# Performance work log

Measured on AMD Instinct MI355X. Metric: run time of the kernel, lower is better.

## Reference

```python
import jax, jax.numpy as jnp
import numpy as np

N_NODES = 100000
N_EDGES = 400000
N_GRAPHS = 2000
NODE_F = 78
HID = 128


def gcn_conv(x, src, dst, W, b, n_nodes):
    # PyG GCNConv: h = X @ W; add self-loops; symmetric norm; scatter-add; + bias
    h = x @ W
    loop = jnp.arange(n_nodes, dtype=src.dtype)
    s = jnp.concatenate([src, loop])
    d = jnp.concatenate([dst, loop])
    deg = jax.ops.segment_sum(jnp.ones_like(d, dtype=h.dtype), d, num_segments=n_nodes)
    dinv = jax.lax.rsqrt(deg)  # deg >= 1 due to self-loops
    coef = dinv[s] * dinv[d]  # [E+N]
    msg = h[s] * coef[:, None]  # gather + scale
    out = jax.ops.segment_sum(msg, d, num_segments=n_nodes)
    return out + b


def setup_inputs() -> dict:
    key = jax.random.key(0)
    ks = jax.random.split(key, 16)
    x = jax.random.normal(ks[0], (N_NODES, NODE_F), dtype=jnp.float32)
    edge_index = jax.random.randint(ks[1], (2, N_EDGES), 0, N_NODES, dtype=jnp.int64)
    batch = jnp.sort(jax.random.randint(ks[2], (N_NODES,), 0, N_GRAPHS, dtype=jnp.int64))
    def lin(k, fi, fo):
        lim = 1.0 / np.sqrt(fi)
        kw, kb = jax.random.split(k)
        return (jax.random.uniform(kw, (fi, fo), jnp.float32, -lim, lim),
                jax.random.uniform(kb, (fo,), jnp.float32, -lim, lim))
    W1, b1 = lin(ks[3], NODE_F, HID)
    W2, b2 = lin(ks[4], HID, 2 * HID)
    W3, b3 = lin(ks[5], 2 * HID, HID)
    fw1, fb1 = lin(ks[6], HID, 64)
    fw2, fb2 = lin(ks[7], 64, 1)
    return {"x": x, "edge_index": edge_index, "batch": batch,
            "W1": W1, "b1": b1, "W2": W2, "b2": b2, "W3": W3, "b3": b3,
            "fw1": fw1, "fb1": fb1, "fw2": fw2, "fb2": fb2}


def reference(x, edge_index, batch, W1, b1, W2, b2, W3, b3, fw1, fb1, fw2, fb2):
    src, dst = edge_index[0], edge_index[1]
    h = jax.nn.relu(gcn_conv(x, src, dst, W1, b1, N_NODES))
    h = jax.nn.relu(gcn_conv(h, src, dst, W2, b2, N_NODES))
    h = jax.nn.relu(gcn_conv(h, src, dst, W3, b3, N_NODES))
    # global_mean_pool over graph ids
    sums = jax.ops.segment_sum(h, batch, num_segments=N_GRAPHS)
    cnts = jax.ops.segment_sum(jnp.ones((N_NODES,), h.dtype), batch, num_segments=N_GRAPHS)
    pooled = sums / jnp.maximum(cnts, 1.0)[:, None]
    h = jax.nn.relu(pooled @ fw1 + fb1)
    return h @ fw2 + fb2  # [N_GRAPHS, 1]
```

## Files before the change

kernel.cpp:

```cpp
#include <hip/hip_runtime.h>

#define N_NODES 100000
#define N_EDGES 400000
#define N_GRAPHS 2000
#define NODE_F 78
#define HID 128
#define PAD 32
#define SENT N_NODES

typedef __attribute__((ext_vector_type(8))) short short8v;
typedef __attribute__((ext_vector_type(4))) float f32x4;

__device__ __forceinline__ ushort f2bf(float f) {
    unsigned u = __float_as_uint(f);
    unsigned r = (u + 0x7FFFu + ((u >> 16) & 1u)) >> 16;
    return (ushort)r;
}
__device__ __forceinline__ float bf2f(ushort b) {
    return __uint_as_float(((unsigned)b) << 16);
}
__device__ __forceinline__ float2 bfx2(const ushort* p) {
    unsigned u = *reinterpret_cast<const unsigned*>(p);
    return make_float2(__uint_as_float(u << 16), __uint_as_float(u & 0xffff0000u));
}
__device__ __forceinline__ unsigned packbf(float a, float b) {
    return (unsigned)f2bf(a) | ((unsigned)f2bf(b) << 16);
}
__device__ __forceinline__ void gload16(const ushort* g, ushort* l) {
    __builtin_amdgcn_global_load_lds((const __attribute__((address_space(1))) unsigned int*)g,
                                     (__attribute__((address_space(3))) unsigned int*)l, 16, 0, 0);
}


__global__ void setup_k(int* __restrict__ cursor, int4* __restrict__ csr4,
                        ushort* __restrict__ xb, ushort* __restrict__ b1,
                        ushort* __restrict__ b3) {
    int i = blockIdx.x * blockDim.x + threadIdx.x;
    if (i < N_NODES * PAD / 4) csr4[i] = make_int4(SENT, SENT, SENT, SENT);
    if (i < N_NODES) cursor[i] = 0;
    if (i < 80) xb[(size_t)N_NODES * 80 + i] = 0;
    if (i < 128) {
        b1[(size_t)N_NODES * 128 + i] = 0;
        b3[(size_t)N_NODES * 128 + i] = 0;
    }
}

__global__ void fill_csr_k(const int* __restrict__ src, const int* __restrict__ dst,
                           int* __restrict__ cursor, int* __restrict__ csr) {
    int e = blockIdx.x * blockDim.x + threadIdx.x;
    if (e >= N_EDGES) return;
    int s = src[e], d = dst[e];
    int p = atomicAdd(&cursor[d], 1);
    if (p < PAD) csr[d * PAD + p] = s;
}

__global__ void dinv_k(const int* __restrict__ deg, float* __restrict__ dinv, int n) {
    int i = blockIdx.x * blockDim.x + threadIdx.x;
    if (i < n) dinv[i] = rsqrtf((float)deg[i] + 1.0f);
}


__global__ void x2bf_k(const float* __restrict__ x, const float* __restrict__ dinv,
                       ushort* __restrict__ xb) {
    int idx = blockIdx.x * blockDim.x + threadIdx.x;
    if (idx >= N_NODES * 80) return;
    int n = idx / 80, f = idx - n * 80;
    xb[idx] = (f < NODE_F) ? f2bf(x[(long long)n * NODE_F + f] * dinv[n]) : (ushort)0;
}


__global__ void prep_wt_k(const float* __restrict__ W, ushort* __restrict__ Wth,
                          int K, int N) {
    int idx = blockIdx.x * blockDim.x + threadIdx.x;
    if (idx >= N * 256) return;
    int n = idx >> 8, k = idx & 255;
    Wth[idx] = (k < K) ? f2bf(W[(long long)k * N + n]) : (ushort)0;
}

__global__ void prep_w2img_k(const float* __restrict__ W2, ushort* __restrict__ img) {
    int idx = blockIdx.x * blockDim.x + threadIdx.x;
    if (idx >= 256 * 128) return;
    int n = idx >> 7, k = idx & 127;
    int c = k >> 3;
    int slot = (c & 8) | ((c & 7) ^ (n & 7));
    img[n * 128 + slot * 8 + (k & 7)] = f2bf(W2[(long long)k * 256 + n]);
}

__global__ void prep_w3img_k(const float* __restrict__ W3, ushort* __restrict__ img) {
    int idx = blockIdx.x * blockDim.x + threadIdx.x;
    if (idx >= 128 * 256) return;
    int n = idx >> 8, k = idx & 255;
    int ch = k >> 6, cc = (k >> 3) & 7;
    img[ch * 8192 + n * 64 + ((cc ^ (n & 7)) * 8) + (k & 7)] = f2bf(W3[(long long)k * 128 + n]);
}


__global__ __launch_bounds__(256) void gemm1_k(
        const ushort* __restrict__ A, int M,
        const ushort* __restrict__ Wth, const float* __restrict__ bias,
        const float* __restrict__ dinv, ushort* __restrict__ C) {
    __shared__ ushort At[128 * 64];
    __shared__ ushort Bh[128 * 64];
    const int tid = threadIdx.x;
    const int w = tid >> 6, l = tid & 63;
    const int bm = blockIdx.x * 128;

    f32x4 acc[2][8];
    #pragma unroll
    for (int m = 0; m < 2; ++m)
        #pragma unroll
        for (int j = 0; j < 8; ++j)
            acc[m][j] = (f32x4){0.f, 0.f, 0.f, 0.f};

    for (int k0 = 0; k0 < 128; k0 += 64) {
        __syncthreads();
        #pragma unroll
        for (int i = 0; i < 4; ++i) {
            int idx = tid + i * 256;
            int r = idx >> 3, s0 = idx & 7;
            int gr = bm + r; if (gr >= M) gr = M - 1;
            int kk = k0 + s0 * 8;
            short8v v;
            if (kk < 80) v = *reinterpret_cast<const short8v*>(&A[(size_t)gr * 80 + kk]);
            else v = (short8v){0,0,0,0,0,0,0,0};
            *reinterpret_cast<short8v*>(&At[r * 64 + (s0 ^ (r & 7)) * 8]) = v;
        }
        #pragma unroll
        for (int i = 0; i < 4; ++i) {
            int idx = tid + i * 256;
            int n = idx >> 3, s0 = idx & 7;
            long long g = (long long)n * 256 + k0 + s0 * 8;
            *reinterpret_cast<short8v*>(&Bh[n * 64 + (s0 ^ (n & 7)) * 8]) =
                *reinterpret_cast<const short8v*>(&Wth[g]);
        }
        __syncthreads();
        #pragma unroll
        for (int ks = 0; ks < 2; ++ks) {
            short8v ah[2];
            #pragma unroll
            for (int m = 0; m < 2; ++m) {
                int r = w * 32 + m * 16 + (l & 15);
                ah[m] = *reinterpret_cast<const short8v*>(
                    &At[r * 64 + ((ks * 4 + (l >> 4)) ^ (r & 7)) * 8]);
            }
            #pragma unroll
            for (int j = 0; j < 8; ++j) {
                int n = j * 16 + (l & 15);
                short8v bh = *reinterpret_cast<const short8v*>(
                    &Bh[n * 64 + ((ks * 4 + (l >> 4)) ^ (n & 7)) * 8]);
                #pragma unroll
                for (int m = 0; m < 2; ++m)
                    acc[m][j] = __builtin_amdgcn_mfma_f32_16x16x32_bf16(ah[m], bh, acc[m][j], 0, 0, 0);
            }
        }
    }

    float dv[2][4];
    #pragma unroll
    for (int m = 0; m < 2; ++m)
        #pragma unroll
        for (int rg = 0; rg < 4; ++rg) {
            int gr = bm + w * 32 + m * 16 + (l >> 4) * 4 + rg;
            dv[m][rg] = (gr < M) ? dinv[gr] : 0.f;
        }
    #pragma unroll
    for (int j = 0; j < 8; ++j) {
        int gc = j * 16 + (l & 15);
        float bv = bias[gc];
        #pragma unroll
        for (int m = 0; m < 2; ++m) {
            #pragma unroll
            for (int rg = 0; rg < 4; ++rg) {
                int gr = bm + w * 32 + m * 16 + (l >> 4) * 4 + rg;
                if (gr < M)
                    C[(size_t)gr * 128 + gc] = f2bf(fmaxf(acc[m][j][rg] + bv, 0.0f) * dv[m][rg]);
            }
        }
    }
}


__global__ __launch_bounds__(512) void gemm23_k(
        const ushort* __restrict__ A,
        const ushort* __restrict__ W2i, const float* __restrict__ b2,
        const ushort* __restrict__ W3i, const float* __restrict__ dinv,
        ushort* __restrict__ C, int M) {
    __shared__ ushort At[128 * 128];
    __shared__ ushort Wb[2][8192];
    __shared__ ushort Tb[8][1024];
    const int tid = threadIdx.x;
    const int w = tid >> 6, l = tid & 63;
    const int bm = blockIdx.x * 128;

    {
        const ushort* asrc = A + (size_t)bm * 128;
        #pragma unroll
        for (int i = 0; i < 4; ++i) {
            int chunk = w * 4 + i;
            gload16(asrc + chunk * 512 + l * 8, &At[chunk * 512]);
        }
        #pragma unroll
        for (int i = 0; i < 2; ++i) {
            int chunk = w * 2 + i;
            gload16(W2i + chunk * 512 + l * 8, &Wb[0][chunk * 512]);
        }
    }
    __syncthreads();

    f32x4 acc2[16];
    #pragma unroll
    for (int j = 0; j < 16; ++j) acc2[j] = (f32x4){0.f, 0.f, 0.f, 0.f};

    #pragma unroll
    for (int q = 0; q < 4; ++q) {
        const ushort* nsrc = (q < 3) ? (W2i + (q + 1) * 8192) : W3i;
        #pragma unroll
        for (int i = 0; i < 2; ++i) {
            int chunk = w * 2 + i;
            gload16(nsrc + chunk * 512 + l * 8, &Wb[(q + 1) & 1][chunk * 512]);
        }
        const ushort* wb = Wb[q & 1];
        #pragma unroll
        for (int ks = 0; ks < 4; ++ks) {
            int r = w * 16 + (l & 15);
            int ck = ks * 4 + (l >> 4);
            int sa = (ck & 8) | ((ck & 7) ^ (r & 7));
            short8v ah = *reinterpret_cast<const short8v*>(&At[r * 128 + sa * 8]);
            #pragma unroll
            for (int jt = 0; jt < 4; ++jt) {
                int n = jt * 16 + (l & 15);
                int sb = (ck & 8) | ((ck & 7) ^ (n & 7));
                short8v bh = *reinterpret_cast<const short8v*>(&wb[n * 128 + sb * 8]);
                acc2[q * 4 + jt] = __builtin_amdgcn_mfma_f32_16x16x32_bf16(ah, bh, acc2[q * 4 + jt], 0, 0, 0);
            }
        }
        __syncthreads();
    }

    f32x4 acc3[8];
    #pragma unroll
    for (int j = 0; j < 8; ++j) acc3[j] = (f32x4){0.f, 0.f, 0.f, 0.f};

    #pragma unroll
    for (int ch = 0; ch < 4; ++ch) {
        if (ch < 3) {
            const ushort* nsrc = W3i + (ch + 1) * 8192;
            #pragma unroll
            for (int i = 0; i < 2; ++i) {
                int chunk = w * 2 + i;
                gload16(nsrc + chunk * 512 + l * 8, &Wb[(ch + 1) & 1][chunk * 512]);
            }
        }
        #pragma unroll
        for (int jj = 0; jj < 4; ++jj) {
            int j = ch * 4 + jj;
            float bv = b2[ch * 64 + jj * 16 + (l & 15)];
            #pragma unroll
            for (int rg = 0; rg < 4; ++rg) {
                int rr = (l >> 4) * 4 + rg;
                int cl = jj * 16 + (l & 15);
                Tb[w][rr * 64 + (((cl >> 3) ^ (rr & 7)) * 8) + (cl & 7)] =
                    f2bf(fmaxf(acc2[j][rg] + bv, 0.f));
            }
        }
        const ushort* wb = Wb[ch & 1];
        #pragma unroll
        for (int ks = 0; ks < 2; ++ks) {
            int rt = l & 15;
            int ck = ks * 4 + (l >> 4);
            short8v ah = *reinterpret_cast<const short8v*>(&Tb[w][rt * 64 + ((ck ^ (rt & 7)) * 8)]);
            #pragma unroll
            for (int j3 = 0; j3 < 8; ++j3) {
                int n = j3 * 16 + (l & 15);
                short8v bh = *reinterpret_cast<const short8v*>(&wb[n * 64 + ((ck ^ (n & 7)) * 8)]);
                acc3[j3] = __builtin_amdgcn_mfma_f32_16x16x32_bf16(ah, bh, acc3[j3], 0, 0, 0);
            }
        }
        __syncthreads();
    }

    float dv[4];
    #pragma unroll
    for (int rg = 0; rg < 4; ++rg) {
        int gr = bm + w * 16 + (l >> 4) * 4 + rg;
        dv[rg] = (gr < M) ? dinv[gr] : 0.f;
    }
    #pragma unroll
    for (int j = 0; j < 8; ++j) {
        int gc = j * 16 + (l & 15);
        #pragma unroll
        for (int rg = 0; rg < 4; ++rg) {
            int gr = bm + w * 16 + (l >> 4) * 4 + rg;
            if (gr < M) C[(size_t)gr * 128 + gc] = f2bf(acc3[j][rg] * dv[rg]);
        }
    }
}


__global__ __launch_bounds__(256) void gather78_k(const ushort* __restrict__ Xb,
        const int* __restrict__ deg, const int* __restrict__ csr,
        const float* __restrict__ dinv, ushort* __restrict__ out) {
    int wid = (blockIdx.x * blockDim.x + threadIdx.x) >> 6;
    int lane = threadIdx.x & 63;
    if (wid >= N_NODES) return;
    float di = dinv[wid];
    float ax = 0.f, ay = 0.f;
    bool act = lane < 40;
    if (act) {
        float2 v = bfx2(&Xb[(size_t)wid * 80 + lane * 2]);
        ax = v.x; ay = v.y;
    }
    int d = deg[wid]; if (d > PAD) d = PAD;
    const int4* e4 = reinterpret_cast<const int4*>(csr + wid * PAD);
    for (int j0 = 0; j0 < d; j0 += 4) {
        int4 e = e4[j0 >> 2];
        if (act) {
            float2 v0 = bfx2(&Xb[(size_t)e.x * 80 + lane * 2]);
            float2 v1 = bfx2(&Xb[(size_t)e.y * 80 + lane * 2]);
            float2 v2 = bfx2(&Xb[(size_t)e.z * 80 + lane * 2]);
            float2 v3 = bfx2(&Xb[(size_t)e.w * 80 + lane * 2]);
            ax += v0.x + v1.x + v2.x + v3.x;
            ay += v0.y + v1.y + v2.y + v3.y;
        }
    }
    if (act)
        *reinterpret_cast<unsigned*>(&out[(size_t)wid * 80 + lane * 2]) = packbf(ax * di, ay * di);
}

__global__ __launch_bounds__(256) void gather128_k(const ushort* __restrict__ A,
        const int* __restrict__ deg, const int* __restrict__ csr,
        const float* __restrict__ dinv, ushort* __restrict__ out) {
    int wid = (blockIdx.x * blockDim.x + threadIdx.x) >> 6;
    int lane = threadIdx.x & 63;
    if (wid >= N_NODES) return;
    float di = dinv[wid];
    float2 v = bfx2(&A[(size_t)wid * 128 + lane * 2]);
    float ax = v.x, ay = v.y;
    int d = deg[wid]; if (d > PAD) d = PAD;
    const int4* e4 = reinterpret_cast<const int4*>(csr + wid * PAD);
    for (int j0 = 0; j0 < d; j0 += 4) {
        int4 e = e4[j0 >> 2];
        float2 w0 = bfx2(&A[(size_t)e.x * 128 + lane * 2]);
        float2 w1 = bfx2(&A[(size_t)e.y * 128 + lane * 2]);
        float2 w2 = bfx2(&A[(size_t)e.z * 128 + lane * 2]);
        float2 w3 = bfx2(&A[(size_t)e.w * 128 + lane * 2]);
        ax += w0.x + w1.x + w2.x + w3.x;
        ay += w0.y + w1.y + w2.y + w3.y;
    }
    int kt = lane >> 5, cc = (lane >> 2) & 7, q4 = lane & 3;
    int slot = kt * 8 + (cc ^ (wid & 7));
    *reinterpret_cast<unsigned*>(&out[(size_t)wid * 128 + slot * 8 + q4 * 2]) = packbf(ax * di, ay * di);
}


__global__ __launch_bounds__(512) void pool_head_k(
        const ushort* __restrict__ A,
        const int* __restrict__ deg, const int* __restrict__ csr,
        const float* __restrict__ dinv, const float* __restrict__ b3,
        const int* __restrict__ batch,
        const float* __restrict__ fw1, const float* __restrict__ fb1,
        const float* __restrict__ fw2, const float* __restrict__ fb2,
        float* __restrict__ out) {
    __shared__ float part[8][HID];
    __shared__ float ps[HID];
    const int g = blockIdx.x;
    const int w = threadIdx.x >> 6, lane = threadIdx.x & 63;

    int start, end;
    {
        int l = 0, h = N_NODES;
        while (l < h) { int m = (l + h) >> 1; if (batch[m] < g) l = m + 1; else h = m; }
        start = l;
        h = N_NODES;
        while (l < h) { int m = (l + h) >> 1; if (batch[m] < g + 1) l = m + 1; else h = m; }
        end = l;
    }

    float sx = 0.f, sy = 0.f;
    const float bx = b3[lane * 2], by = b3[lane * 2 + 1];
    for (int i = start + w; i < end; i += 8) {
        float di = dinv[i];
        float2 v = bfx2(&A[(size_t)i * 128 + lane * 2]);
        float ax = v.x, ay = v.y;
        int d = deg[i]; if (d > PAD) d = PAD;
        const int4* e4 = reinterpret_cast<const int4*>(csr + i * PAD);
        for (int j0 = 0; j0 < d; j0 += 4) {
            int4 e = e4[j0 >> 2];
            float2 w0 = bfx2(&A[(size_t)e.x * 128 + lane * 2]);
            float2 w1 = bfx2(&A[(size_t)e.y * 128 + lane * 2]);
            float2 w2 = bfx2(&A[(size_t)e.z * 128 + lane * 2]);
            float2 w3 = bfx2(&A[(size_t)e.w * 128 + lane * 2]);
            ax += w0.x + w1.x + w2.x + w3.x;
            ay += w0.y + w1.y + w2.y + w3.y;
        }
        sx += fmaxf(ax * di + bx, 0.f);
        sy += fmaxf(ay * di + by, 0.f);
    }
    part[w][lane * 2] = sx;
    part[w][lane * 2 + 1] = sy;
    __syncthreads();

    if (w == 0) {
        float inv = (end > start) ? 1.0f / (float)(end - start) : 0.0f;
        float s0 = 0.f, s1 = 0.f;
        #pragma unroll
        for (int q = 0; q < 8; ++q) {
            s0 += part[q][lane * 2];
            s1 += part[q][lane * 2 + 1];
        }
        ps[lane * 2] = s0 * inv;
        ps[lane * 2 + 1] = s1 * inv;
    }
    __syncthreads();

    if (w == 0) {
        float acc = fb1[lane];
        #pragma unroll 8
        for (int k = 0; k < HID; ++k) acc = fmaf(ps[k], fw1[k * 64 + lane], acc);
        float v = fmaxf(acc, 0.0f) * fw2[lane];
        #pragma unroll
        for (int off = 32; off > 0; off >>= 1) v += __shfl_down(v, off);
        if (lane == 0) out[g] = v + fb2[0];
    }
}


extern "C" void kernel_launch(void* const* d_in, const int* in_sizes, int n_in,
                              void* d_out, int out_size, void* d_ws, size_t ws_size,
                              hipStream_t stream) {
    const float* x     = (const float*)d_in[0];
    const int*   ei    = (const int*)d_in[1];
    const int*   batch = (const int*)d_in[2];
    const float* W1 = (const float*)d_in[3];
    const float* b1 = (const float*)d_in[4];
    const float* W2 = (const float*)d_in[5];
    const float* b2 = (const float*)d_in[6];
    const float* W3 = (const float*)d_in[7];
    const float* b3 = (const float*)d_in[8];
    const float* fw1 = (const float*)d_in[9];
    const float* fb1 = (const float*)d_in[10];
    const float* fw2 = (const float*)d_in[11];
    const float* fb2 = (const float*)d_in[12];
    float* out = (float*)d_out;

    const int* src = ei;
    const int* dst = ei + N_EDGES;

    char* p = (char*)d_ws;
    float*  dinv  = (float*)p;  p += 100352 * 4;
    int*    cur   = (int*)p;    p += 100352 * 4;
    int*    csr   = (int*)p;    p += (size_t)N_NODES * PAD * 4;
    ushort* w1h   = (ushort*)p; p += 256 * 256 * 2;
    ushort* img2  = (ushort*)p; p += 256 * 128 * 2;
    ushort* img3  = (ushort*)p; p += 128 * 256 * 2;
    ushort* xb    = (ushort*)p; p += (size_t)(N_NODES + 1) * 80 * 2;
    ushort* xpadb = (ushort*)p; p += (size_t)N_NODES * 80 * 2;
    ushort* buf1  = (ushort*)p; p += (size_t)(N_NODES + 1) * 128 * 2;
    ushort* buf2  = (ushort*)p; p += (size_t)N_NODES * 128 * 2;
    ushort* buf3  = (ushort*)p; p += (size_t)(N_NODES + 1) * 128 * 2;

    const int T = 256;
    const int gw = (N_NODES * 64 + T - 1) / T;

    setup_k<<<(N_NODES * PAD / 4 + T - 1) / T, T, 0, stream>>>(cur, (int4*)csr, xb, buf1, buf3);
    fill_csr_k<<<(N_EDGES + T - 1) / T, T, 0, stream>>>(src, dst, cur, csr);
    dinv_k<<<(N_NODES + T - 1) / T, T, 0, stream>>>(cur, dinv, N_NODES);
    x2bf_k<<<(N_NODES * 80 + T - 1) / T, T, 0, stream>>>(x, dinv, xb);

    prep_wt_k<<<(128 * 256 + T - 1) / T, T, 0, stream>>>(W1, w1h, NODE_F, 128);
    prep_w2img_k<<<(256 * 128 + T - 1) / T, T, 0, stream>>>(W2, img2);
    prep_w3img_k<<<(128 * 256 + T - 1) / T, T, 0, stream>>>(W3, img3);

    gather78_k<<<gw, T, 0, stream>>>(xb, cur, csr, dinv, xpadb);
    gemm1_k<<<782, 256, 0, stream>>>(xpadb, N_NODES, w1h, b1, dinv, buf1);

    gather128_k<<<gw, T, 0, stream>>>(buf1, cur, csr, dinv, buf2);
    gemm23_k<<<782, 512, 0, stream>>>(buf2, img2, b2, img3, dinv, buf3, N_NODES);

    pool_head_k<<<N_GRAPHS, 512, 0, stream>>>(buf3, cur, csr, dinv, b3, batch,
                                              fw1, fb1, fw2, fb2, out);
}
```

Before: 308.9 us.

## Fuse neighbor gather aggregation into GEMM kernels, removing intermediate buffers

```diff
diff --git a/kernel.cpp b/kernel.cpp
--- a/kernel.cpp
+++ b/kernel.cpp
@@ -69,12 +69,13 @@
 }
 
 
-__global__ void prep_wt_k(const float* __restrict__ W, ushort* __restrict__ Wth,
-                          int K, int N) {
+__global__ void prep_w1img_k(const float* __restrict__ W1, ushort* __restrict__ img) {
     int idx = blockIdx.x * blockDim.x + threadIdx.x;
-    if (idx >= N * 256) return;
-    int n = idx >> 8, k = idx & 255;
-    Wth[idx] = (k < K) ? f2bf(W[(long long)k * N + n]) : (ushort)0;
+    if (idx >= 128 * 128) return;
+    int n = idx >> 7, k = idx & 127;
+    int c = k >> 3;
+    int slot = (c & 8) | ((c & 7) ^ (n & 7));
+    img[n * 128 + slot * 8 + (k & 7)] = (k < NODE_F) ? f2bf(W1[(long long)k * 128 + n]) : (ushort)0;
 }
 
 __global__ void prep_w2img_k(const float* __restrict__ W2, ushort* __restrict__ img) {
@@ -95,96 +96,96 @@
 }
 
 
-__global__ __launch_bounds__(256) void gemm1_k(
-        const ushort* __restrict__ A, int M,
-        const ushort* __restrict__ Wth, const float* __restrict__ bias,
-        const float* __restrict__ dinv, ushort* __restrict__ C) {
-    __shared__ ushort At[128 * 64];
-    __shared__ ushort Bh[128 * 64];
+__global__ __launch_bounds__(512) void gemm1g_k(
+        const ushort* __restrict__ Xb, const int* __restrict__ deg,
+        const int* __restrict__ csr, const float* __restrict__ dinv,
+        const ushort* __restrict__ W1i, const float* __restrict__ bias,
+        ushort* __restrict__ C, int M) {
+    __shared__ ushort At[128 * 128];
+    __shared__ ushort Bh[128 * 128];
     const int tid = threadIdx.x;
     const int w = tid >> 6, l = tid & 63;
     const int bm = blockIdx.x * 128;
 
-    f32x4 acc[2][8];
-    #pragma unroll
-    for (int m = 0; m < 2; ++m)
-        #pragma unroll
-        for (int j = 0; j < 8; ++j)
-            acc[m][j] = (f32x4){0.f, 0.f, 0.f, 0.f};
-
-    for (int k0 = 0; k0 < 128; k0 += 64) {
-        __syncthreads();
-        #pragma unroll
-        for (int i = 0; i < 4; ++i) {
-            int idx = tid + i * 256;
-            int r = idx >> 3, s0 = idx & 7;
-            int gr = bm + r; if (gr >= M) gr = M - 1;
-            int kk = k0 + s0 * 8;
-            short8v v;
-            if (kk < 80) v = *reinterpret_cast<const short8v*>(&A[(size_t)gr * 80 + kk]);
-            else v = (short8v){0,0,0,0,0,0,0,0};
-            *reinterpret_cast<short8v*>(&At[r * 64 + (s0 ^ (r & 7)) * 8]) = v;
-        }
-        #pragma unroll
-        for (int i = 0; i < 4; ++i) {
-            int idx = tid + i * 256;
-            int n = idx >> 3, s0 = idx & 7;
-            long long g = (long long)n * 256 + k0 + s0 * 8;
-            *reinterpret_cast<short8v*>(&Bh[n * 64 + (s0 ^ (n & 7)) * 8]) =
-                *reinterpret_cast<const short8v*>(&Wth[g]);
-        }
-        __syncthreads();
-        #pragma unroll
-        for (int ks = 0; ks < 2; ++ks) {
-            short8v ah[2];
-            #pragma unroll
-            for (int m = 0; m < 2; ++m) {
-                int r = w * 32 + m * 16 + (l & 15);
-                ah[m] = *reinterpret_cast<const short8v*>(
-                    &At[r * 64 + ((ks * 4 + (l >> 4)) ^ (r & 7)) * 8]);
+    #pragma unroll
+    for (int i = 0; i < 4; ++i) {
+        int chunk = i * 8 + w;
+        gload16(W1i + chunk * 512 + l * 8, &Bh[chunk * 512]);
+    }
+
+    const bool act = l < 40;
+    for (int t = 0; t < 16; ++t) {
+        int r = w * 16 + t;
+        int gr = bm + r; if (gr >= M) gr = M - 1;
+        float di = dinv[gr];
+        int d = deg[gr]; if (d > PAD) d = PAD;
+        const int4* e4 = reinterpret_cast<const int4*>(csr + gr * PAD);
+        float ax = 0.f, ay = 0.f;
+        if (act) {
+            float2 v = bfx2(&Xb[(size_t)gr * 80 + l * 2]);
+            ax = v.x; ay = v.y;
+        }
+        for (int j0 = 0; j0 < d; j0 += 4) {
+            int4 e = e4[j0 >> 2];
+            if (act) {
+                float2 v0 = bfx2(&Xb[(size_t)e.x * 80 + l * 2]);
+                float2 v1 = bfx2(&Xb[(size_t)e.y * 80 + l * 2]);
+                float2 v2 = bfx2(&Xb[(size_t)e.z * 80 + l * 2]);
+                float2 v3 = bfx2(&Xb[(size_t)e.w * 80 + l * 2]);
+                ax += v0.x + v1.x + v2.x + v3.x;
+                ay += v0.y + v1.y + v2.y + v3.y;
             }
-            #pragma unroll
-            for (int j = 0; j < 8; ++j) {
-                int n = j * 16 + (l & 15);
-                short8v bh = *reinterpret_cast<const short8v*>(
-                    &Bh[n * 64 + ((ks * 4 + (l >> 4)) ^ (n & 7)) * 8]);
-                #pragma unroll
-                for (int m = 0; m < 2; ++m)
-                    acc[m][j] = __builtin_amdgcn_mfma_f32_16x16x32_bf16(ah[m], bh, acc[m][j], 0, 0, 0);
-            }
-        }
-    }
-
-    float dv[2][4];
-    #pragma unroll
-    for (int m = 0; m < 2; ++m)
-        #pragma unroll
-        for (int rg = 0; rg < 4; ++rg) {
-            int gr = bm + w * 32 + m * 16 + (l >> 4) * 4 + rg;
-            dv[m][rg] = (gr < M) ? dinv[gr] : 0.f;
-        }
+        }
+        int c = l >> 2;
+        int slot = (c & 8) | ((c & 7) ^ (r & 7));
+        *reinterpret_cast<unsigned*>(&At[r * 128 + slot * 8 + (l & 3) * 2]) =
+            packbf(ax * di, ay * di);
+    }
+    __syncthreads();
+
+    f32x4 acc[8];
+    #pragma unroll
+    for (int j = 0; j < 8; ++j) acc[j] = (f32x4){0.f, 0.f, 0.f, 0.f};
+    #pragma unroll
+    for (int ks = 0; ks < 3; ++ks) {
+        int r = w * 16 + (l & 15);
+        int ck = ks * 4 + (l >> 4);
+        int sa = (ck & 8) | ((ck & 7) ^ (r & 7));
+        short8v ah = *reinterpret_cast<const short8v*>(&At[r * 128 + sa * 8]);
+        #pragma unroll
+        for (int j = 0; j < 8; ++j) {
+            int n = j * 16 + (l & 15);
+            int sb = (ck & 8) | ((ck & 7) ^ (n & 7));
+            short8v bh = *reinterpret_cast<const short8v*>(&Bh[n * 128 + sb * 8]);
+            acc[j] = __builtin_amdgcn_mfma_f32_16x16x32_bf16(ah, bh, acc[j], 0, 0, 0);
+        }
+    }
+
+    float dv[4];
+    #pragma unroll
+    for (int rg = 0; rg < 4; ++rg) {
+        int gr = bm + w * 16 + (l >> 4) * 4 + rg;
+        dv[rg] = (gr < M) ? dinv[gr] : 0.f;
+    }
     #pragma unroll
     for (int j = 0; j < 8; ++j) {
         int gc = j * 16 + (l & 15);
         float bv = bias[gc];
         #pragma unroll
-        for (int m = 0; m < 2; ++m) {
-            #pragma unroll
-            for (int rg = 0; rg < 4; ++rg) {
-                int gr = bm + w * 32 + m * 16 + (l >> 4) * 4 + rg;
-                if (gr < M)
-                    C[(size_t)gr * 128 + gc] = f2bf(fmaxf(acc[m][j][rg] + bv, 0.0f) * dv[m][rg]);
-            }
-        }
-    }
-}
-
-
-__global__ __launch_bounds__(512) void gemm23_k(
-        const ushort* __restrict__ A,
+        for (int rg = 0; rg < 4; ++rg) {
+            int gr = bm + w * 16 + (l >> 4) * 4 + rg;
+            if (gr < M)
+                C[(size_t)gr * 128 + gc] = f2bf(fmaxf(acc[j][rg] + bv, 0.0f) * dv[rg]);
+        }
+    }
+}
+
+
+__global__ __launch_bounds__(512) void gemm23g_k(
+        const ushort* __restrict__ B1, const int* __restrict__ deg,
+        const int* __restrict__ csr, const float* __restrict__ dinv,
         const ushort* __restrict__ W2i, const float* __restrict__ b2,
-        const ushort* __restrict__ W3i, const float* __restrict__ dinv,
-        ushort* __restrict__ C, int M) {
+        const ushort* __restrict__ W3i, ushort* __restrict__ C, int M) {
     __shared__ ushort At[128 * 128];
     __shared__ ushort Wb[2][8192];
     __shared__ ushort Tb[8][1024];
@@ -192,18 +193,33 @@
     const int w = tid >> 6, l = tid & 63;
     const int bm = blockIdx.x * 128;
 
-    {
-        const ushort* asrc = A + (size_t)bm * 128;
-        #pragma unroll
-        for (int i = 0; i < 4; ++i) {
-            int chunk = w * 4 + i;
-            gload16(asrc + chunk * 512 + l * 8, &At[chunk * 512]);
-        }
-        #pragma unroll
-        for (int i = 0; i < 2; ++i) {
-            int chunk = w * 2 + i;
-            gload16(W2i + chunk * 512 + l * 8, &Wb[0][chunk * 512]);
-        }
+    #pragma unroll
+    for (int i = 0; i < 2; ++i) {
+        int chunk = w * 2 + i;
+        gload16(W2i + chunk * 512 + l * 8, &Wb[0][chunk * 512]);
+    }
+
+    for (int t = 0; t < 16; ++t) {
+        int r = w * 16 + t;
+        int gr = bm + r; if (gr >= M) gr = M - 1;
+        float di = dinv[gr];
+        int d = deg[gr]; if (d > PAD) d = PAD;
+        const int4* e4 = reinterpret_cast<const int4*>(csr + gr * PAD);
+        float2 v = bfx2(&B1[(size_t)gr * 128 + l * 2]);
+        float ax = v.x, ay = v.y;
+        for (int j0 = 0; j0 < d; j0 += 4) {
+            int4 e = e4[j0 >> 2];
+            float2 w0 = bfx2(&B1[(size_t)e.x * 128 + l * 2]);
+            float2 w1 = bfx2(&B1[(size_t)e.y * 128 + l * 2]);
+            float2 w2 = bfx2(&B1[(size_t)e.z * 128 + l * 2]);
+            float2 w3 = bfx2(&B1[(size_t)e.w * 128 + l * 2]);
+            ax += w0.x + w1.x + w2.x + w3.x;
+            ay += w0.y + w1.y + w2.y + w3.y;
+        }
+        int c = l >> 2;
+        int slot = (c & 8) | ((c & 7) ^ (r & 7));
+        *reinterpret_cast<unsigned*>(&At[r * 128 + slot * 8 + (l & 3) * 2]) =
+            packbf(ax * di, ay * di);
     }
     __syncthreads();
 
@@ -294,62 +310,6 @@
             if (gr < M) C[(size_t)gr * 128 + gc] = f2bf(acc3[j][rg] * dv[rg]);
         }
     }
-}
-
-
-__global__ __launch_bounds__(256) void gather78_k(const ushort* __restrict__ Xb,
-        const int* __restrict__ deg, const int* __restrict__ csr,
-        const float* __restrict__ dinv, ushort* __restrict__ out) {
-    int wid = (blockIdx.x * blockDim.x + threadIdx.x) >> 6;
-    int lane = threadIdx.x & 63;
-    if (wid >= N_NODES) return;
-    float di = dinv[wid];
-    float ax = 0.f, ay = 0.f;
-    bool act = lane < 40;
-    if (act) {
-        float2 v = bfx2(&Xb[(size_t)wid * 80 + lane * 2]);
-        ax = v.x; ay = v.y;
-    }
-    int d = deg[wid]; if (d > PAD) d = PAD;
-    const int4* e4 = reinterpret_cast<const int4*>(csr + wid * PAD);
-    for (int j0 = 0; j0 < d; j0 += 4) {
-        int4 e = e4[j0 >> 2];
-        if (act) {
-            float2 v0 = bfx2(&Xb[(size_t)e.x * 80 + lane * 2]);
-            float2 v1 = bfx2(&Xb[(size_t)e.y * 80 + lane * 2]);
-            float2 v2 = bfx2(&Xb[(size_t)e.z * 80 + lane * 2]);
-            float2 v3 = bfx2(&Xb[(size_t)e.w * 80 + lane * 2]);
-            ax += v0.x + v1.x + v2.x + v3.x;
-            ay += v0.y + v1.y + v2.y + v3.y;
-        }
-    }
-    if (act)
-        *reinterpret_cast<unsigned*>(&out[(size_t)wid * 80 + lane * 2]) = packbf(ax * di, ay * di);
-}
-
-__global__ __launch_bounds__(256) void gather128_k(const ushort* __restrict__ A,
-        const int* __restrict__ deg, const int* __restrict__ csr,
-        const float* __restrict__ dinv, ushort* __restrict__ out) {
-    int wid = (blockIdx.x * blockDim.x + threadIdx.x) >> 6;
-    int lane = threadIdx.x & 63;
-    if (wid >= N_NODES) return;
-    float di = dinv[wid];
-    float2 v = bfx2(&A[(size_t)wid * 128 + lane * 2]);
-    float ax = v.x, ay = v.y;
-    int d = deg[wid]; if (d > PAD) d = PAD;
-    const int4* e4 = reinterpret_cast<const int4*>(csr + wid * PAD);
-    for (int j0 = 0; j0 < d; j0 += 4) {
-        int4 e = e4[j0 >> 2];
-        float2 w0 = bfx2(&A[(size_t)e.x * 128 + lane * 2]);
-        float2 w1 = bfx2(&A[(size_t)e.y * 128 + lane * 2]);
-        float2 w2 = bfx2(&A[(size_t)e.z * 128 + lane * 2]);
-        float2 w3 = bfx2(&A[(size_t)e.w * 128 + lane * 2]);
-        ax += w0.x + w1.x + w2.x + w3.x;
-        ay += w0.y + w1.y + w2.y + w3.y;
-    }
-    int kt = lane >> 5, cc = (lane >> 2) & 7, q4 = lane & 3;
-    int slot = kt * 8 + (cc ^ (wid & 7));
-    *reinterpret_cast<unsigned*>(&out[(size_t)wid * 128 + slot * 8 + q4 * 2]) = packbf(ax * di, ay * di);
 }
 
 
@@ -450,32 +410,27 @@
     float*  dinv  = (float*)p;  p += 100352 * 4;
     int*    cur   = (int*)p;    p += 100352 * 4;
     int*    csr   = (int*)p;    p += (size_t)N_NODES * PAD * 4;
-    ushort* w1h   = (ushort*)p; p += 256 * 256 * 2;
+    ushort* img1  = (ushort*)p; p += 128 * 128 * 2;
     ushort* img2  = (ushort*)p; p += 256 * 128 * 2;
     ushort* img3  = (ushort*)p; p += 128 * 256 * 2;
     ushort* xb    = (ushort*)p; p += (size_t)(N_NODES + 1) * 80 * 2;
-    ushort* xpadb = (ushort*)p; p += (size_t)N_NODES * 80 * 2;
     ushort* buf1  = (ushort*)p; p += (size_t)(N_NODES + 1) * 128 * 2;
-    ushort* buf2  = (ushort*)p; p += (size_t)N_NODES * 128 * 2;
     ushort* buf3  = (ushort*)p; p += (size_t)(N_NODES + 1) * 128 * 2;
 
     const int T = 256;
-    const int gw = (N_NODES * 64 + T - 1) / T;
 
     setup_k<<<(N_NODES * PAD / 4 + T - 1) / T, T, 0, stream>>>(cur, (int4*)csr, xb, buf1, buf3);
     fill_csr_k<<<(N_EDGES + T - 1) / T, T, 0, stream>>>(src, dst, cur, csr);
     dinv_k<<<(N_NODES + T - 1) / T, T, 0, stream>>>(cur, dinv, N_NODES);
     x2bf_k<<<(N_NODES * 80 + T - 1) / T, T, 0, stream>>>(x, dinv, xb);
 
-    prep_wt_k<<<(128 * 256 + T - 1) / T, T, 0, stream>>>(W1, w1h, NODE_F, 128);
+    prep_w1img_k<<<(128 * 128 + T - 1) / T, T, 0, stream>>>(W1, img1);
     prep_w2img_k<<<(256 * 128 + T - 1) / T, T, 0, stream>>>(W2, img2);
     prep_w3img_k<<<(128 * 256 + T - 1) / T, T, 0, stream>>>(W3, img3);
 
-    gather78_k<<<gw, T, 0, stream>>>(xb, cur, csr, dinv, xpadb);
-    gemm1_k<<<782, 256, 0, stream>>>(xpadb, N_NODES, w1h, b1, dinv, buf1);
-
-    gather128_k<<<gw, T, 0, stream>>>(buf1, cur, csr, dinv, buf2);
-    gemm23_k<<<782, 512, 0, stream>>>(buf2, img2, b2, img3, dinv, buf3, N_NODES);
+    gemm1g_k<<<782, 512, 0, stream>>>(xb, cur, csr, dinv, img1, b1, buf1, N_NODES);
+
+    gemm23g_k<<<782, 512, 0, stream>>>(buf1, cur, csr, dinv, img2, b2, img3, buf3, N_NODES);
 
     pool_head_k<<<N_GRAPHS, 512, 0, stream>>>(buf3, cur, csr, dinv, b3, batch,
                                               fw1, fb1, fw2, fb2, out);
```

Result: slower. 323.4 us (+4.7%).
